# Kernel tuning notes

Measured on AMD Instinct MI355X. Metric: run time of the kernel, lower is better.

## Reference

```python
import jax, jax.numpy as jnp
import numpy as np

N = 512          # num_satellites
STATE_DIM = 6    # pos(3) + vel(3)
OBJ_DIM = 58
F = STATE_DIM + OBJ_DIM          # node feature dim = 64
HID = (128, 64, 32)
EDGE_IN = 2 * F + 1              # sender + receiver + distance
NODE_IN = F + HID[-1]            # node feats + aggregated messages


def _linear_init(key, d_in, d_out):
    kw, _ = jax.random.split(key)
    w = jax.random.normal(kw, (d_in, d_out), jnp.float32) / np.sqrt(d_in).astype(np.float32)
    b = jnp.zeros((d_out,), jnp.float32)
    return w, b


def setup_inputs() -> dict:
    key = jax.random.key(0)
    ks = jax.random.split(key, 12)
    ew0, eb0 = _linear_init(ks[0], EDGE_IN, HID[0])
    ew1, eb1 = _linear_init(ks[1], HID[0], HID[1])
    ew2, eb2 = _linear_init(ks[2], HID[1], HID[2])
    nw0, nb0 = _linear_init(ks[3], NODE_IN, HID[0])
    nw1, nb1 = _linear_init(ks[4], HID[0], HID[1])
    nw2, nb2 = _linear_init(ks[5], HID[1], HID[2])
    nwo, nbo = _linear_init(ks[6], HID[2], F)   # residual projection back to F
    rw, rb = _linear_init(ks[7], F, 3)          # control readout
    states = jax.random.normal(ks[8], (N, STATE_DIM), jnp.float32)
    objectives = jax.random.normal(ks[9], (OBJ_DIM,), jnp.float32)
    return dict(states=states, objectives=objectives,
                ew0=ew0, eb0=eb0, ew1=ew1, eb1=eb1, ew2=ew2, eb2=eb2,
                nw0=nw0, nb0=nb0, nw1=nw1, nb1=nb1, nw2=nw2, nb2=nb2,
                nwo=nwo, nbo=nbo, rw=rw, rb=rb,
                num_message_passing=3)


def _edge_index(n):
    ii, jj = np.meshgrid(np.arange(n), np.arange(n), indexing='ij')
    m = ii != jj
    return jnp.asarray(ii[m]), jnp.asarray(jj[m])  # sender i, receiver j; E = n*(n-1)


def reference(states, objectives, ew0, eb0, ew1, eb1, ew2, eb2,
              nw0, nb0, nw1, nb1, nw2, nb2, nwo, nbo, rw, rb,
              num_message_passing):
    n = states.shape[0]
    snd, rcv = _edge_index(n)
    # node features: state concat broadcast objectives -> [N, F]
    nf = jnp.concatenate(
        [states, jnp.broadcast_to(objectives, (n, objectives.shape[0]))], axis=-1)
    # distances from raw states (constant across iterations): [E, 1]
    rel = states[rcv, :3] - states[snd, :3]
    dist = jnp.linalg.norm(rel, axis=-1, keepdims=True)
    relu = jax.nn.relu
    for _ in range(num_message_passing):
        # edge MLP over all E edges: [E, 2F+1] -> [E, 32]
        x = jnp.concatenate([nf[snd], nf[rcv], dist], axis=-1)
        h = relu(x @ ew0 + eb0)
        h = relu(h @ ew1 + eb1)
        msg = relu(h @ ew2 + eb2)
        # sum-aggregate incoming messages at receiver j: [N, 32]
        agg = jax.ops.segment_sum(msg, rcv, num_segments=n)
        # node MLP + residual: [N, F+32] -> [N, F]
        y = jnp.concatenate([nf, agg], axis=-1)
        h = relu(y @ nw0 + nb0)
        h = relu(h @ nw1 + nb1)
        h = relu(h @ nw2 + nb2)
        nf = nf + h @ nwo + nbo
    # control readout: [N, 3]
    return nf @ rw + rb
```

## Files before the change

kernel.cpp:

```cpp
#include <hip/hip_runtime.h>
#include <math.h>

#define NSAT 512
#define FDIM 64
#define H0D  128
#define H1D  64
#define H2D  32
#define KP1  68
#define ROWS 256

#define WS_NF    0
#define WS_PSA   (WS_NF  + NSAT * FDIM)
#define WS_PRA   (WS_PSA + NSAT * H0D)
#define WS_PSB   (WS_PRA + NSAT * H0D)
#define WS_PRB   (WS_PSB + NSAT * H0D)
#define WS_WT    (WS_PRB + NSAT * H0D)

using short8_t = __attribute__((ext_vector_type(8))) short;
using short4_t = __attribute__((ext_vector_type(4))) short;
using int4_t   = __attribute__((ext_vector_type(4))) int;
using int2_t   = __attribute__((ext_vector_type(2))) int;
using floatx4  = __attribute__((ext_vector_type(4))) float;
using floatx16 = __attribute__((ext_vector_type(16))) float;

__device__ __forceinline__ void split_ru(float x, short& hi, short& lo) {
    unsigned u = __builtin_bit_cast(unsigned, x);
    unsigned hb = (u + 0x8000u) >> 16;
    hi = (short)hb;
    float r = x - __builtin_bit_cast(float, hb << 16);
    lo = (short)((__builtin_bit_cast(unsigned, r) + 0x8000u) >> 16);
}

__device__ __forceinline__ void split8_pk(const float* __restrict__ v,
                                          short8_t& bh, short8_t& bl) {
    unsigned t[8]; unsigned ru[8];
    #pragma unroll
    for (int e = 0; e < 8; ++e) {
        unsigned u = __builtin_bit_cast(unsigned, v[e]);
        t[e] = u + 0x8000u;
        float r = v[e] - __builtin_bit_cast(float, t[e] & 0xffff0000u);
        ru[e] = __builtin_bit_cast(unsigned, r);
    }
    int4_t hv, lv;
    #pragma unroll
    for (int p = 0; p < 4; ++p) {
        hv[p] = (int)__builtin_amdgcn_perm(t[2*p+1],  t[2*p],  0x07060302u);
        lv[p] = (int)__builtin_amdgcn_perm(ru[2*p+1], ru[2*p], 0x07060302u);
    }
    bh = __builtin_bit_cast(short8_t, hv);
    bl = __builtin_bit_cast(short8_t, lv);
}

__device__ __forceinline__ void split4_pk(const float* __restrict__ v,
                                          short4_t& h, short4_t& l) {
    unsigned t[4]; unsigned ru[4];
    #pragma unroll
    for (int e = 0; e < 4; ++e) {
        unsigned u = __builtin_bit_cast(unsigned, v[e]);
        t[e] = u + 0x8000u;
        float r = v[e] - __builtin_bit_cast(float, t[e] & 0xffff0000u);
        ru[e] = __builtin_bit_cast(unsigned, r);
    }
    int2_t hv, lv;
    #pragma unroll
    for (int p = 0; p < 2; ++p) {
        hv[p] = (int)__builtin_amdgcn_perm(t[2*p+1],  t[2*p],  0x07060302u);
        lv[p] = (int)__builtin_amdgcn_perm(ru[2*p+1], ru[2*p], 0x07060302u);
    }
    h = __builtin_bit_cast(short4_t, hv);
    l = __builtin_bit_cast(short4_t, lv);
}

__device__ __forceinline__ void compute_pre(const float* __restrict__ nfl,
                                            const float* __restrict__ ew0,
                                            const float* __restrict__ eb0,
                                            int i, int t,
                                            float* __restrict__ preSA,
                                            float* __restrict__ preR) {
    if (t < H0D) {
        int k = t;
        float s0 = 0.f, s1 = 0.f, s2 = 0.f, s3 = 0.f;
        #pragma unroll
        for (int f = 0; f < FDIM; f += 4) {
            s0 = fmaf(nfl[f + 0], ew0[(f + 0) * H0D + k], s0);
            s1 = fmaf(nfl[f + 1], ew0[(f + 1) * H0D + k], s1);
            s2 = fmaf(nfl[f + 2], ew0[(f + 2) * H0D + k], s2);
            s3 = fmaf(nfl[f + 3], ew0[(f + 3) * H0D + k], s3);
        }
        int kk = (k >> 3) & 7, lhi = k >> 6, jj = k & 7;
        preSA[((i >> 5) * 8 + kk) * 512 + (lhi * 32 + (i & 31)) * 8 + jj] =
            (s0 + s1) + (s2 + s3);
    } else if (t < 2 * H0D) {
        int k = t - H0D;
        float s0 = eb0[k], s1 = 0.f, s2 = 0.f, s3 = 0.f;
        #pragma unroll
        for (int f = 0; f < FDIM; f += 4) {
            s0 = fmaf(nfl[f + 0], ew0[(FDIM + f + 0) * H0D + k], s0);
            s1 = fmaf(nfl[f + 1], ew0[(FDIM + f + 1) * H0D + k], s1);
            s2 = fmaf(nfl[f + 2], ew0[(FDIM + f + 2) * H0D + k], s2);
            s3 = fmaf(nfl[f + 3], ew0[(FDIM + f + 3) * H0D + k], s3);
        }
        preR[i * H0D + k] = (s0 + s1) + (s2 + s3);
    }
}

__global__ void setup_kernel(const float* __restrict__ states,
                             const float* __restrict__ objectives,
                             const float* __restrict__ ew0,
                             const float* __restrict__ eb0,
                             const float* __restrict__ ew1,
                             const float* __restrict__ ew2,
                             float* __restrict__ nf,
                             float* __restrict__ preSA,
                             float* __restrict__ preR,
                             short* __restrict__ w1A_hi,
                             short* __restrict__ w1A_lo,
                             short* __restrict__ w2t_hi,
                             short* __restrict__ w2t_lo) {
    __shared__ float nfl[FDIM];
    int b = blockIdx.x, t = threadIdx.x;
    if (b < NSAT) {
        if (t < FDIM) {
            float v = (t < 6) ? states[b * 6 + t] : objectives[t - 6];
            nfl[t] = v;
            nf[b * FDIM + t] = v;
        }
        __syncthreads();
        compute_pre(nfl, ew0, eb0, b, t, preSA, preR);
    } else {
        int e = (b - NSAT) * 256 + t;
        if (e < H1D * H0D) {
            int jj = e & 7;
            int l  = (e >> 3) & 63;
            int kk = (e >> 9) & 7;
            int mh = e >> 12;
            int m = mh * 32 + (l & 31);
            int k = (l >> 5) * 64 + kk * 8 + jj;
            short hi, lo; split_ru(ew1[k * H1D + m], hi, lo);
            w1A_hi[e] = hi; w1A_lo[e] = lo;
        } else if (e < H1D * H0D + H2D * H1D) {
            int e2 = e - H1D * H0D;
            int c = e2 >> 6, k = e2 & 63;
            short hi, lo; split_ru(ew2[k * H2D + c], hi, lo);
            w2t_hi[e2] = hi; w2t_lo[e2] = lo;
        }
    }
}

__global__ __launch_bounds__(512, 2)
void edge_node_kernel(const float* __restrict__ states,
                      const float* __restrict__ preSA,
                      const float* __restrict__ preR,
                      const float* __restrict__ ew0,
                      const float* __restrict__ eb0,
                      const float* __restrict__ eb1,
                      const float* __restrict__ eb2,
                      const short* __restrict__ w1A_hi,
                      const short* __restrict__ w1A_lo,
                      const short* __restrict__ w2t_hi,
                      const short* __restrict__ w2t_lo,
                      const float* __restrict__ nw0, const float* __restrict__ nb0,
                      const float* __restrict__ nw1, const float* __restrict__ nb1,
                      const float* __restrict__ nw2, const float* __restrict__ nb2,
                      const float* __restrict__ nwo, const float* __restrict__ nbo,
                      const float* __restrict__ rw,  const float* __restrict__ rb,
                      float* __restrict__ nf,
                      float* __restrict__ preSA_w,
                      float* __restrict__ preR_w,
                      float* __restrict__ out,
                      int final_iter) {
    extern __shared__ __align__(16) short h1_dyn[];
    short* h1_hi = h1_dyn;
    short* h1_lo = h1_dyn + ROWS * KP1;

    __shared__ __align__(16) float preR_l[H0D];
    __shared__ __align__(16) float wd_l[H0D];
    __shared__ __align__(16) float eb1_l[H1D];
    __shared__ float eb2_l[H2D];
    __shared__ __align__(16) float red_l[8 * H2D];
    __shared__ float y_l[96];
    __shared__ float hA_l[H0D];
    __shared__ float hB_l[H1D];
    __shared__ float hC_l[H2D];
    __shared__ float nfl2[FDIM];

    int t = threadIdx.x, j = blockIdx.x;
    int w = t >> 6, lane = t & 63;
    int lhi = lane >> 5, llo = lane & 31;

    if (t < H0D)                          preR_l[t] = preR[j * H0D + t];
    else if (t < 2 * H0D)                 wd_l[t - H0D] = ew0[H0D * H0D + (t - H0D)];
    else if (t < 2 * H0D + H1D)           eb1_l[t - 2 * H0D] = eb1[t - 2 * H0D];
    else if (t < 2 * H0D + H1D + H2D)     eb2_l[t - 2 * H0D - H1D] = eb2[t - 2 * H0D - H1D];
    __syncthreads();

    float rjx = states[j * 6 + 0];
    float rjy = states[j * 6 + 1];
    float rjz = states[j * 6 + 2];

    int s_loc = w * 32 + llo;
    const short* pAh0 = w1A_hi + lane * 8;
    const short* pAl0 = w1A_lo + lane * 8;

    int lq = lane >> 4, l15 = lane & 15;
    const short* pA2h0 = w2t_hi + l15 * H1D + lq * 8;
    const short* pA2l0 = w2t_lo + l15 * H1D + lq * 8;
    const short* pA2h1 = w2t_hi + (16 + l15) * H1D + lq * 8;
    const short* pA2l1 = w2t_lo + (16 + l15) * H1D + lq * 8;
    int boA = (w * 32 + l15) * KP1 + lq * 8;
    int boB = boA + 16 * KP1;

    float racc[8];
    #pragma unroll
    for (int r = 0; r < 8; ++r) racc[r] = 0.f;

    #pragma unroll 1
    for (int P = 0; P < 2; ++P) {
        int s_glb = P * ROWS + s_loc;
        float dx = states[s_glb * 6 + 0] - rjx;
        float dy = states[s_glb * 6 + 1] - rjy;
        float dz = states[s_glb * 6 + 2] - rjz;
        float d = sqrtf(dx * dx + dy * dy + dz * dz);

        const float* pS = preSA + (size_t)((P * 8 + w) * 8) * 512 + lane * 8;

        floatx16 accA, accB;
        #pragma unroll
        for (int r = 0; r < 16; ++r) { accA[r] = 0.f; accB[r] = 0.f; }

        #pragma unroll
        for (int kk = 0; kk < 8; ++kk) {
            float4 a0 = *(const float4*)(pS + kk * 512);
            float4 a1 = *(const float4*)(pS + kk * 512 + 4);
            int kb = lhi * 64 + kk * 8;
            float4 r0 = *(const float4*)&preR_l[kb];
            float4 r1 = *(const float4*)&preR_l[kb + 4];
            float4 q0 = *(const float4*)&wd_l[kb];
            float4 q1 = *(const float4*)&wd_l[kb + 4];
            float v[8];
            v[0] = fmaxf(a0.x + fmaf(d, q0.x, r0.x), 0.f);
            v[1] = fmaxf(a0.y + fmaf(d, q0.y, r0.y), 0.f);
            v[2] = fmaxf(a0.z + fmaf(d, q0.z, r0.z), 0.f);
            v[3] = fmaxf(a0.w + fmaf(d, q0.w, r0.w), 0.f);
            v[4] = fmaxf(a1.x + fmaf(d, q1.x, r1.x), 0.f);
            v[5] = fmaxf(a1.y + fmaf(d, q1.y, r1.y), 0.f);
            v[6] = fmaxf(a1.z + fmaf(d, q1.z, r1.z), 0.f);
            v[7] = fmaxf(a1.w + fmaf(d, q1.w, r1.w), 0.f);
            short8_t bh, bl;
            split8_pk(v, bh, bl);
            short8_t ah0 = *(const short8_t*)(pAh0 + kk * 512);
            short8_t al0 = *(const short8_t*)(pAl0 + kk * 512);
            short8_t ah1 = *(const short8_t*)(pAh0 + 4096 + kk * 512);
            short8_t al1 = *(const short8_t*)(pAl0 + 4096 + kk * 512);
            accA = __builtin_amdgcn_mfma_f32_32x32x16_bf16(ah0, bh, accA, 0, 0, 0);
            accA = __builtin_amdgcn_mfma_f32_32x32x16_bf16(ah0, bl, accA, 0, 0, 0);
            accA = __builtin_amdgcn_mfma_f32_32x32x16_bf16(al0, bh, accA, 0, 0, 0);
            accB = __builtin_amdgcn_mfma_f32_32x32x16_bf16(ah1, bh, accB, 0, 0, 0);
            accB = __builtin_amdgcn_mfma_f32_32x32x16_bf16(ah1, bl, accB, 0, 0, 0);
            accB = __builtin_amdgcn_mfma_f32_32x32x16_bf16(al1, bh, accB, 0, 0, 0);
        }

        asm volatile("s_waitcnt lgkmcnt(0)" ::: "memory");

        {
            #pragma unroll
            for (int mh = 0; mh < 2; ++mh) {
                #pragma unroll
                for (int q = 0; q < 4; ++q) {
                    int m0 = mh * 32 + q * 8 + lhi * 4;
                    float vv[4];
                    #pragma unroll
                    for (int r = 0; r < 4; ++r) {
                        float c = mh ? accB[q * 4 + r] : accA[q * 4 + r];
                        vv[r] = fmaxf(c + eb1_l[m0 + r], 0.f);
                    }
                    short4_t ph, pl;
                    split4_pk(vv, ph, pl);
                    *(short4_t*)&h1_hi[s_loc * KP1 + m0] = ph;
                    *(short4_t*)&h1_lo[s_loc * KP1 + m0] = pl;
                }
            }
        }

        floatx4 aA0, aA1, aB0, aB1;
        #pragma unroll
        for (int r = 0; r < 4; ++r) { aA0[r]=0.f; aA1[r]=0.f; aB0[r]=0.f; aB1[r]=0.f; }
        #pragma unroll
        for (int kk = 0; kk < 2; ++kk) {
            short4_t b0, b1, c0, c1;
            b0 = *(const short4_t*)&h1_hi[boA + kk * 32];
            b1 = *(const short4_t*)&h1_hi[boA + kk * 32 + 4];
            c0 = *(const short4_t*)&h1_lo[boA + kk * 32];
            c1 = *(const short4_t*)&h1_lo[boA + kk * 32 + 4];
            short8_t bhA = __builtin_shufflevector(b0, b1, 0,1,2,3,4,5,6,7);
            short8_t blA = __builtin_shufflevector(c0, c1, 0,1,2,3,4,5,6,7);
            b0 = *(const short4_t*)&h1_hi[boB + kk * 32];
            b1 = *(const short4_t*)&h1_hi[boB + kk * 32 + 4];
            c0 = *(const short4_t*)&h1_lo[boB + kk * 32];
            c1 = *(const short4_t*)&h1_lo[boB + kk * 32 + 4];
            short8_t bhB = __builtin_shufflevector(b0, b1, 0,1,2,3,4,5,6,7);
            short8_t blB = __builtin_shufflevector(c0, c1, 0,1,2,3,4,5,6,7);
            short8_t a0h = *(const short8_t*)(pA2h0 + kk * 32);
            short8_t a0l = *(const short8_t*)(pA2l0 + kk * 32);
            short8_t a1h = *(const short8_t*)(pA2h1 + kk * 32);
            short8_t a1l = *(const short8_t*)(pA2l1 + kk * 32);
            aA0 = __builtin_amdgcn_mfma_f32_16x16x32_bf16(a0h, bhA, aA0, 0, 0, 0);
            aA0 = __builtin_amdgcn_mfma_f32_16x16x32_bf16(a0h, blA, aA0, 0, 0, 0);
            aA0 = __builtin_amdgcn_mfma_f32_16x16x32_bf16(a0l, bhA, aA0, 0, 0, 0);
            aA1 = __builtin_amdgcn_mfma_f32_16x16x32_bf16(a1h, bhA, aA1, 0, 0, 0);
            aA1 = __builtin_amdgcn_mfma_f32_16x16x32_bf16(a1h, blA, aA1, 0, 0, 0);
            aA1 = __builtin_amdgcn_mfma_f32_16x16x32_bf16(a1l, bhA, aA1, 0, 0, 0);
            aB0 = __builtin_amdgcn_mfma_f32_16x16x32_bf16(a0h, bhB, aB0, 0, 0, 0);
            aB0 = __builtin_amdgcn_mfma_f32_16x16x32_bf16(a0h, blB, aB0, 0, 0, 0);
            aB0 = __builtin_amdgcn_mfma_f32_16x16x32_bf16(a0l, bhB, aB0, 0, 0, 0);
            aB1 = __builtin_amdgcn_mfma_f32_16x16x32_bf16(a1h, bhB, aB1, 0, 0, 0);
            aB1 = __builtin_amdgcn_mfma_f32_16x16x32_bf16(a1h, blB, aB1, 0, 0, 0);
            aB1 = __builtin_amdgcn_mfma_f32_16x16x32_bf16(a1l, bhB, aB1, 0, 0, 0);
        }

        {
            bool selfA = (P * ROWS + w * 32 + l15 == j);
            bool selfB = (P * ROWS + w * 32 + 16 + l15 == j);
            #pragma unroll
            for (int r = 0; r < 4; ++r) {
                float vA = fmaxf(aA0[r] + eb2_l[lq * 4 + r], 0.f);
                float vB = fmaxf(aB0[r] + eb2_l[lq * 4 + r], 0.f);
                if (selfA) vA = 0.f;
                if (selfB) vB = 0.f;
                racc[r] += vA + vB;
                float wA = fmaxf(aA1[r] + eb2_l[16 + lq * 4 + r], 0.f);
                float wB = fmaxf(aB1[r] + eb2_l[16 + lq * 4 + r], 0.f);
                if (selfA) wA = 0.f;
                if (selfB) wB = 0.f;
                racc[4 + r] += wA + wB;
            }
        }
    }

    {
        #pragma unroll
        for (int r = 0; r < 8; ++r) {
            float v = racc[r];
            v += __shfl_xor(v, 1, 64); v += __shfl_xor(v, 2, 64);
            v += __shfl_xor(v, 4, 64); v += __shfl_xor(v, 8, 64);
            racc[r] = v;
        }
        if (l15 == 0) {
            *(float4*)&red_l[w * H2D + lq * 4] =
                make_float4(racc[0], racc[1], racc[2], racc[3]);
            *(float4*)&red_l[w * H2D + 16 + lq * 4] =
                make_float4(racc[4], racc[5], racc[6], racc[7]);
        }
    }
    __syncthreads();

    if (t < FDIM) y_l[t] = nf[j * FDIM + t];
    else if (t < 96) {
        int c = t - FDIM;
        float s = 0.f;
        #pragma unroll
        for (int gg = 0; gg < 8; ++gg) s += red_l[gg * H2D + c];
        y_l[t] = s;
    }
    __syncthreads();
    if (t < H0D) {
        float s0 = nb0[t], s1 = 0.f, s2 = 0.f, s3 = 0.f;
        #pragma unroll
        for (int f = 0; f < 96; f += 4) {
            s0 = fmaf(y_l[f + 0], nw0[(f + 0) * H0D + t], s0);
            s1 = fmaf(y_l[f + 1], nw0[(f + 1) * H0D + t], s1);
            s2 = fmaf(y_l[f + 2], nw0[(f + 2) * H0D + t], s2);
            s3 = fmaf(y_l[f + 3], nw0[(f + 3) * H0D + t], s3);
        }
        hA_l[t] = fmaxf((s0 + s1) + (s2 + s3), 0.f);
    }
    __syncthreads();
    if (t < H1D) {
        float s0 = nb1[t], s1 = 0.f, s2 = 0.f, s3 = 0.f;
        #pragma unroll
        for (int k = 0; k < H0D; k += 4) {
            s0 = fmaf(hA_l[k + 0], nw1[(k + 0) * H1D + t], s0);
            s1 = fmaf(hA_l[k + 1], nw1[(k + 1) * H1D + t], s1);
            s2 = fmaf(hA_l[k + 2], nw1[(k + 2) * H1D + t], s2);
            s3 = fmaf(hA_l[k + 3], nw1[(k + 3) * H1D + t], s3);
        }
        hB_l[t] = fmaxf((s0 + s1) + (s2 + s3), 0.f);
    }
    __syncthreads();
    if (t < H2D) {
        float s0 = nb2[t], s1 = 0.f, s2 = 0.f, s3 = 0.f;
        #pragma unroll
        for (int m = 0; m < H1D; m += 4) {
            s0 = fmaf(hB_l[m + 0], nw2[(m + 0) * H2D + t], s0);
            s1 = fmaf(hB_l[m + 1], nw2[(m + 1) * H2D + t], s1);
            s2 = fmaf(hB_l[m + 2], nw2[(m + 2) * H2D + t], s2);
            s3 = fmaf(hB_l[m + 3], nw2[(m + 3) * H2D + t], s3);
        }
        hC_l[t] = fmaxf((s0 + s1) + (s2 + s3), 0.f);
    }
    __syncthreads();
    if (t < FDIM) {
        float s = nbo[t];
        #pragma unroll
        for (int c = 0; c < H2D; ++c) s = fmaf(hC_l[c], nwo[c * FDIM + t], s);
        float v = y_l[t] + s;
        nfl2[t] = v;
        if (!final_iter) nf[j * FDIM + t] = v;
    }
    __syncthreads();
    if (final_iter) {
        if (t < 3) {
            float s0 = rb[t], s1 = 0.f, s2 = 0.f, s3 = 0.f;
            #pragma unroll
            for (int f = 0; f < FDIM; f += 4) {
                s0 = fmaf(nfl2[f + 0], rw[(f + 0) * 3 + t], s0);
                s1 = fmaf(nfl2[f + 1], rw[(f + 1) * 3 + t], s1);
                s2 = fmaf(nfl2[f + 2], rw[(f + 2) * 3 + t], s2);
                s3 = fmaf(nfl2[f + 3], rw[(f + 3) * 3 + t], s3);
            }
            out[j * 3 + t] = (s0 + s1) + (s2 + s3);
        }
    } else {
        compute_pre(nfl2, ew0, eb0, j, t, preSA_w, preR_w);
    }
}

extern "C" void kernel_launch(void* const* d_in, const int* in_sizes, int n_in,
                              void* d_out, int out_size, void* d_ws, size_t ws_size,
                              hipStream_t stream) {
    const float* states     = (const float*)d_in[0];
    const float* objectives = (const float*)d_in[1];
    const float* ew0 = (const float*)d_in[2];
    const float* eb0 = (const float*)d_in[3];
    const float* ew1 = (const float*)d_in[4];
    const float* eb1 = (const float*)d_in[5];
    const float* ew2 = (const float*)d_in[6];
    const float* eb2 = (const float*)d_in[7];
    const float* nw0 = (const float*)d_in[8];
    const float* nb0 = (const float*)d_in[9];
    const float* nw1 = (const float*)d_in[10];
    const float* nb1 = (const float*)d_in[11];
    const float* nw2 = (const float*)d_in[12];
    const float* nb2 = (const float*)d_in[13];
    const float* nwo = (const float*)d_in[14];
    const float* nbo = (const float*)d_in[15];
    const float* rw  = (const float*)d_in[16];
    const float* rb  = (const float*)d_in[17];
    float* out = (float*)d_out;
    float* ws  = (float*)d_ws;

    float* nf      = ws + WS_NF;
    float* preSA_a = ws + WS_PSA;
    float* preR_a  = ws + WS_PRA;
    float* preSA_b = ws + WS_PSB;
    float* preR_b  = ws + WS_PRB;
    short* w1A_hi = (short*)(ws + WS_WT);
    short* w1A_lo = w1A_hi + H1D * H0D;
    short* w2t_hi = w1A_lo + H1D * H0D;
    short* w2t_lo = w2t_hi + H2D * H1D;

    const int dyn_lds = 2 * ROWS * KP1 * (int)sizeof(short);
    static bool attr_set = false;
    if (!attr_set) {
        hipFuncSetAttribute((const void*)edge_node_kernel,
                            hipFuncAttributeMaxDynamicSharedMemorySize, dyn_lds);
        attr_set = true;
    }

    setup_kernel<<<NSAT + 40, 256, 0, stream>>>(states, objectives, ew0, eb0,
                                                ew1, ew2, nf, preSA_a, preR_a,
                                                w1A_hi, w1A_lo, w2t_hi, w2t_lo);
    for (int it = 0; it < 3; ++it) {
        const float* pS_r = (it & 1) ? preSA_b : preSA_a;
        const float* pR_r = (it & 1) ? preR_b  : preR_a;
        float* pS_w = (it & 1) ? preSA_a : preSA_b;
        float* pR_w = (it & 1) ? preR_a  : preR_b;
        edge_node_kernel<<<NSAT, 512, dyn_lds, stream>>>(
            states, pS_r, pR_r, ew0, eb0, eb1, eb2,
            w1A_hi, w1A_lo, w2t_hi, w2t_lo,
            nw0, nb0, nw1, nb1, nw2, nb2, nwo, nbo, rw, rb,
            nf, pS_w, pR_w, out, (it == 2) ? 1 : 0);
    }
}
```

Before: 198.1 us.

## Process two receiver nodes per block to reuse sender preactivations and weights

Each block now computes the edge and node MLPs for two receiver nodes, sharing the sender preactivation loads and the bf16 weight fragments across both. The grid is halved, LDS for the hidden layer is doubled, and launch bounds drop to one block per CU. This aims to cut global/L2 traffic and fragment loads per edge, at the cost of more registers, lower occupancy and fewer blocks to balance across CUs.

```diff
diff --git a/kernel.cpp b/kernel.cpp
--- a/kernel.cpp
+++ b/kernel.cpp
@@ -147,7 +147,7 @@
     }
 }
 
-__global__ __launch_bounds__(512, 2)
+__global__ __launch_bounds__(512, 1)
 void edge_node_kernel(const float* __restrict__ states,
                       const float* __restrict__ preSA,
                       const float* __restrict__ preR,
@@ -170,33 +170,36 @@
                       float* __restrict__ out,
                       int final_iter) {
     extern __shared__ __align__(16) short h1_dyn[];
-    short* h1_hi = h1_dyn;
-    short* h1_lo = h1_dyn + ROWS * KP1;
-
-    __shared__ __align__(16) float preR_l[H0D];
+    short* h1_hi0 = h1_dyn;
+    short* h1_lo0 = h1_dyn + ROWS * KP1;
+    short* h1_hi1 = h1_dyn + 2 * ROWS * KP1;
+    short* h1_lo1 = h1_dyn + 3 * ROWS * KP1;
+
+    __shared__ __align__(16) float preR_l[2][H0D];
     __shared__ __align__(16) float wd_l[H0D];
     __shared__ __align__(16) float eb1_l[H1D];
     __shared__ float eb2_l[H2D];
-    __shared__ __align__(16) float red_l[8 * H2D];
-    __shared__ float y_l[96];
-    __shared__ float hA_l[H0D];
-    __shared__ float hB_l[H1D];
-    __shared__ float hC_l[H2D];
-    __shared__ float nfl2[FDIM];
-
-    int t = threadIdx.x, j = blockIdx.x;
+    __shared__ __align__(16) float red_l[2][8 * H2D];
+    __shared__ float y_l[2][96];
+    __shared__ float hA_l[2][H0D];
+    __shared__ float hB_l[2][H1D];
+    __shared__ float hC_l[2][H2D];
+    __shared__ float nfl2[2][FDIM];
+
+    int t = threadIdx.x;
+    int j0 = blockIdx.x * 2, j1 = j0 + 1;
     int w = t >> 6, lane = t & 63;
     int lhi = lane >> 5, llo = lane & 31;
 
-    if (t < H0D)                          preR_l[t] = preR[j * H0D + t];
-    else if (t < 2 * H0D)                 wd_l[t - H0D] = ew0[H0D * H0D + (t - H0D)];
-    else if (t < 2 * H0D + H1D)           eb1_l[t - 2 * H0D] = eb1[t - 2 * H0D];
-    else if (t < 2 * H0D + H1D + H2D)     eb2_l[t - 2 * H0D - H1D] = eb2[t - 2 * H0D - H1D];
-    __syncthreads();
-
-    float rjx = states[j * 6 + 0];
-    float rjy = states[j * 6 + 1];
-    float rjz = states[j * 6 + 2];
+    if (t < H0D)                               preR_l[0][t] = preR[j0 * H0D + t];
+    else if (t < 2 * H0D)                      preR_l[1][t - H0D] = preR[j1 * H0D + (t - H0D)];
+    else if (t < 3 * H0D)                      wd_l[t - 2 * H0D] = ew0[H0D * H0D + (t - 2 * H0D)];
+    else if (t < 3 * H0D + H1D)                eb1_l[t - 3 * H0D] = eb1[t - 3 * H0D];
+    else if (t < 3 * H0D + H1D + H2D)          eb2_l[t - 3 * H0D - H1D] = eb2[t - 3 * H0D - H1D];
+    __syncthreads();
+
+    float r0x = states[j0 * 6 + 0], r0y = states[j0 * 6 + 1], r0z = states[j0 * 6 + 2];
+    float r1x = states[j1 * 6 + 0], r1y = states[j1 * 6 + 1], r1z = states[j1 * 6 + 2];
 
     int s_loc = w * 32 + llo;
     const short* pAh0 = w1A_hi + lane * 8;
@@ -210,59 +213,84 @@
     int boA = (w * 32 + l15) * KP1 + lq * 8;
     int boB = boA + 16 * KP1;
 
-    float racc[8];
+    float racc0[8], racc1[8];
     #pragma unroll
-    for (int r = 0; r < 8; ++r) racc[r] = 0.f;
+    for (int r = 0; r < 8; ++r) { racc0[r] = 0.f; racc1[r] = 0.f; }
 
     #pragma unroll 1
     for (int P = 0; P < 2; ++P) {
         int s_glb = P * ROWS + s_loc;
-        float dx = states[s_glb * 6 + 0] - rjx;
-        float dy = states[s_glb * 6 + 1] - rjy;
-        float dz = states[s_glb * 6 + 2] - rjz;
-        float d = sqrtf(dx * dx + dy * dy + dz * dz);
+        float sx = states[s_glb * 6 + 0];
+        float sy = states[s_glb * 6 + 1];
+        float sz = states[s_glb * 6 + 2];
+        float dx0 = sx - r0x, dy0 = sy - r0y, dz0 = sz - r0z;
+        float d0 = sqrtf(dx0 * dx0 + dy0 * dy0 + dz0 * dz0);
+        float dx1 = sx - r1x, dy1 = sy - r1y, dz1 = sz - r1z;
+        float d1 = sqrtf(dx1 * dx1 + dy1 * dy1 + dz1 * dz1);
 
         const float* pS = preSA + (size_t)((P * 8 + w) * 8) * 512 + lane * 8;
 
-        floatx16 accA, accB;
-        #pragma unroll
-        for (int r = 0; r < 16; ++r) { accA[r] = 0.f; accB[r] = 0.f; }
+        floatx16 accLo0, accHi0, accLo1, accHi1;
+        #pragma unroll
+        for (int r = 0; r < 16; ++r) {
+            accLo0[r] = 0.f; accHi0[r] = 0.f; accLo1[r] = 0.f; accHi1[r] = 0.f;
+        }
 
         #pragma unroll
         for (int kk = 0; kk < 8; ++kk) {
             float4 a0 = *(const float4*)(pS + kk * 512);
             float4 a1 = *(const float4*)(pS + kk * 512 + 4);
             int kb = lhi * 64 + kk * 8;
-            float4 r0 = *(const float4*)&preR_l[kb];
-            float4 r1 = *(const float4*)&preR_l[kb + 4];
+            float4 p00 = *(const float4*)&preR_l[0][kb];
+            float4 p01 = *(const float4*)&preR_l[0][kb + 4];
+            float4 p10 = *(const float4*)&preR_l[1][kb];
+            float4 p11 = *(const float4*)&preR_l[1][kb + 4];
             float4 q0 = *(const float4*)&wd_l[kb];
             float4 q1 = *(const float4*)&wd_l[kb + 4];
-            float v[8];
-            v[0] = fmaxf(a0.x + fmaf(d, q0.x, r0.x), 0.f);
-            v[1] = fmaxf(a0.y + fmaf(d, q0.y, r0.y), 0.f);
-            v[2] = fmaxf(a0.z + fmaf(d, q0.z, r0.z), 0.f);
-            v[3] = fmaxf(a0.w + fmaf(d, q0.w, r0.w), 0.f);
-            v[4] = fmaxf(a1.x + fmaf(d, q1.x, r1.x), 0.f);
-            v[5] = fmaxf(a1.y + fmaf(d, q1.y, r1.y), 0.f);
-            v[6] = fmaxf(a1.z + fmaf(d, q1.z, r1.z), 0.f);
-            v[7] = fmaxf(a1.w + fmaf(d, q1.w, r1.w), 0.f);
-            short8_t bh, bl;
-            split8_pk(v, bh, bl);
-            short8_t ah0 = *(const short8_t*)(pAh0 + kk * 512);
-            short8_t al0 = *(const short8_t*)(pAl0 + kk * 512);
-            short8_t ah1 = *(const short8_t*)(pAh0 + 4096 + kk * 512);
-            short8_t al1 = *(const short8_t*)(pAl0 + 4096 + kk * 512);
-            accA = __builtin_amdgcn_mfma_f32_32x32x16_bf16(ah0, bh, accA, 0, 0, 0);
-            accA = __builtin_amdgcn_mfma_f32_32x32x16_bf16(ah0, bl, accA, 0, 0, 0);
-            accA = __builtin_amdgcn_mfma_f32_32x32x16_bf16(al0, bh, accA, 0, 0, 0);
-            accB = __builtin_amdgcn_mfma_f32_32x32x16_bf16(ah1, bh, accB, 0, 0, 0);
-            accB = __builtin_amdgcn_mfma_f32_32x32x16_bf16(ah1, bl, accB, 0, 0, 0);
-            accB = __builtin_amdgcn_mfma_f32_32x32x16_bf16(al1, bh, accB, 0, 0, 0);
+            float v0[8], v1[8];
+            v0[0] = fmaxf(a0.x + fmaf(d0, q0.x, p00.x), 0.f);
+            v0[1] = fmaxf(a0.y + fmaf(d0, q0.y, p00.y), 0.f);
+            v0[2] = fmaxf(a0.z + fmaf(d0, q0.z, p00.z), 0.f);
+            v0[3] = fmaxf(a0.w + fmaf(d0, q0.w, p00.w), 0.f);
+            v0[4] = fmaxf(a1.x + fmaf(d0, q1.x, p01.x), 0.f);
+            v0[5] = fmaxf(a1.y + fmaf(d0, q1.y, p01.y), 0.f);
+            v0[6] = fmaxf(a1.z + fmaf(d0, q1.z, p01.z), 0.f);
+            v0[7] = fmaxf(a1.w + fmaf(d0, q1.w, p01.w), 0.f);
+            v1[0] = fmaxf(a0.x + fmaf(d1, q0.x, p10.x), 0.f);
+            v1[1] = fmaxf(a0.y + fmaf(d1, q0.y, p10.y), 0.f);
+            v1[2] = fmaxf(a0.z + fmaf(d1, q0.z, p10.z), 0.f);
+            v1[3] = fmaxf(a0.w + fmaf(d1, q0.w, p10.w), 0.f);
+            v1[4] = fmaxf(a1.x + fmaf(d1, q1.x, p11.x), 0.f);
+            v1[5] = fmaxf(a1.y + fmaf(d1, q1.y, p11.y), 0.f);
+            v1[6] = fmaxf(a1.z + fmaf(d1, q1.z, p11.z), 0.f);
+            v1[7] = fmaxf(a1.w + fmaf(d1, q1.w, p11.w), 0.f);
+            short8_t bh0, bl0, bh1, bl1;
+            split8_pk(v0, bh0, bl0);
+            split8_pk(v1, bh1, bl1);
+            short8_t whi0 = *(const short8_t*)(pAh0 + kk * 512);
+            short8_t wlo0 = *(const short8_t*)(pAl0 + kk * 512);
+            short8_t whi1 = *(const short8_t*)(pAh0 + 4096 + kk * 512);
+            short8_t wlo1 = *(const short8_t*)(pAl0 + 4096 + kk * 512);
+            accLo0 = __builtin_amdgcn_mfma_f32_32x32x16_bf16(whi0, bh0, accLo0, 0, 0, 0);
+            accLo1 = __builtin_amdgcn_mfma_f32_32x32x16_bf16(whi0, bh1, accLo1, 0, 0, 0);
+            accHi0 = __builtin_amdgcn_mfma_f32_32x32x16_bf16(whi1, bh0, accHi0, 0, 0, 0);
+            accHi1 = __builtin_amdgcn_mfma_f32_32x32x16_bf16(whi1, bh1, accHi1, 0, 0, 0);
+            accLo0 = __builtin_amdgcn_mfma_f32_32x32x16_bf16(whi0, bl0, accLo0, 0, 0, 0);
+            accLo1 = __builtin_amdgcn_mfma_f32_32x32x16_bf16(whi0, bl1, accLo1, 0, 0, 0);
+            accHi0 = __builtin_amdgcn_mfma_f32_32x32x16_bf16(whi1, bl0, accHi0, 0, 0, 0);
+            accHi1 = __builtin_amdgcn_mfma_f32_32x32x16_bf16(whi1, bl1, accHi1, 0, 0, 0);
+            accLo0 = __builtin_amdgcn_mfma_f32_32x32x16_bf16(wlo0, bh0, accLo0, 0, 0, 0);
+            accLo1 = __builtin_amdgcn_mfma_f32_32x32x16_bf16(wlo0, bh1, accLo1, 0, 0, 0);
+            accHi0 = __builtin_amdgcn_mfma_f32_32x32x16_bf16(wlo1, bh0, accHi0, 0, 0, 0);
+            accHi1 = __builtin_amdgcn_mfma_f32_32x32x16_bf16(wlo1, bh1, accHi1, 0, 0, 0);
         }
 
         asm volatile("s_waitcnt lgkmcnt(0)" ::: "memory");
 
-        {
+        #pragma unroll
+        for (int jx = 0; jx < 2; ++jx) {
+            short* hh = jx ? h1_hi1 : h1_hi0;
+            short* hl = jx ? h1_lo1 : h1_lo0;
             #pragma unroll
             for (int mh = 0; mh < 2; ++mh) {
                 #pragma unroll
@@ -271,68 +299,92 @@
                     float vv[4];
                     #pragma unroll
                     for (int r = 0; r < 4; ++r) {
-                        float c = mh ? accB[q * 4 + r] : accA[q * 4 + r];
+                        float c;
+                        if (jx == 0) c = mh ? accHi0[q * 4 + r] : accLo0[q * 4 + r];
+                        else         c = mh ? accHi1[q * 4 + r] : accLo1[q * 4 + r];
                         vv[r] = fmaxf(c + eb1_l[m0 + r], 0.f);
                     }
                     short4_t ph, pl;
                     split4_pk(vv, ph, pl);
-                    *(short4_t*)&h1_hi[s_loc * KP1 + m0] = ph;
-                    *(short4_t*)&h1_lo[s_loc * KP1 + m0] = pl;
+                    *(short4_t*)&hh[s_loc * KP1 + m0] = ph;
+                    *(short4_t*)&hl[s_loc * KP1 + m0] = pl;
                 }
             }
         }
 
-        floatx4 aA0, aA1, aB0, aB1;
-        #pragma unroll
-        for (int r = 0; r < 4; ++r) { aA0[r]=0.f; aA1[r]=0.f; aB0[r]=0.f; aB1[r]=0.f; }
+        floatx4 aA0_0, aA1_0, aB0_0, aB1_0, aA0_1, aA1_1, aB0_1, aB1_1;
+        #pragma unroll
+        for (int r = 0; r < 4; ++r) {
+            aA0_0[r]=0.f; aA1_0[r]=0.f; aB0_0[r]=0.f; aB1_0[r]=0.f;
+            aA0_1[r]=0.f; aA1_1[r]=0.f; aB0_1[r]=0.f; aB1_1[r]=0.f;
+        }
         #pragma unroll
         for (int kk = 0; kk < 2; ++kk) {
-            short4_t b0, b1, c0, c1;
-            b0 = *(const short4_t*)&h1_hi[boA + kk * 32];
-            b1 = *(const short4_t*)&h1_hi[boA + kk * 32 + 4];
-            c0 = *(const short4_t*)&h1_lo[boA + kk * 32];
-            c1 = *(const short4_t*)&h1_lo[boA + kk * 32 + 4];
-            short8_t bhA = __builtin_shufflevector(b0, b1, 0,1,2,3,4,5,6,7);
-            short8_t blA = __builtin_shufflevector(c0, c1, 0,1,2,3,4,5,6,7);
-            b0 = *(const short4_t*)&h1_hi[boB + kk * 32];
-            b1 = *(const short4_t*)&h1_hi[boB + kk * 32 + 4];
-            c0 = *(const short4_t*)&h1_lo[boB + kk * 32];
-            c1 = *(const short4_t*)&h1_lo[boB + kk * 32 + 4];
-            short8_t bhB = __builtin_shufflevector(b0, b1, 0,1,2,3,4,5,6,7);
-            short8_t blB = __builtin_shufflevector(c0, c1, 0,1,2,3,4,5,6,7);
             short8_t a0h = *(const short8_t*)(pA2h0 + kk * 32);
             short8_t a0l = *(const short8_t*)(pA2l0 + kk * 32);
             short8_t a1h = *(const short8_t*)(pA2h1 + kk * 32);
             short8_t a1l = *(const short8_t*)(pA2l1 + kk * 32);
-            aA0 = __builtin_amdgcn_mfma_f32_16x16x32_bf16(a0h, bhA, aA0, 0, 0, 0);
-            aA0 = __builtin_amdgcn_mfma_f32_16x16x32_bf16(a0h, blA, aA0, 0, 0, 0);
-            aA0 = __builtin_amdgcn_mfma_f32_16x16x32_bf16(a0l, bhA, aA0, 0, 0, 0);
-            aA1 = __builtin_amdgcn_mfma_f32_16x16x32_bf16(a1h, bhA, aA1, 0, 0, 0);
-            aA1 = __builtin_amdgcn_mfma_f32_16x16x32_bf16(a1h, blA, aA1, 0, 0, 0);
-            aA1 = __builtin_amdgcn_mfma_f32_16x16x32_bf16(a1l, bhA, aA1, 0, 0, 0);
-            aB0 = __builtin_amdgcn_mfma_f32_16x16x32_bf16(a0h, bhB, aB0, 0, 0, 0);
-            aB0 = __builtin_amdgcn_mfma_f32_16x16x32_bf16(a0h, blB, aB0, 0, 0, 0);
-            aB0 = __builtin_amdgcn_mfma_f32_16x16x32_bf16(a0l, bhB, aB0, 0, 0, 0);
-            aB1 = __builtin_amdgcn_mfma_f32_16x16x32_bf16(a1h, bhB, aB1, 0, 0, 0);
-            aB1 = __builtin_amdgcn_mfma_f32_16x16x32_bf16(a1h, blB, aB1, 0, 0, 0);
-            aB1 = __builtin_amdgcn_mfma_f32_16x16x32_bf16(a1l, bhB, aB1, 0, 0, 0);
+            #pragma unroll
+            for (int jx = 0; jx < 2; ++jx) {
+                const short* hh = jx ? h1_hi1 : h1_hi0;
+                const short* hl = jx ? h1_lo1 : h1_lo0;
+                short4_t u0, u1, c0, c1;
+                u0 = *(const short4_t*)&hh[boA + kk * 32];
+                u1 = *(const short4_t*)&hh[boA + kk * 32 + 4];
+                c0 = *(const short4_t*)&hl[boA + kk * 32];
+                c1 = *(const short4_t*)&hl[boA + kk * 32 + 4];
+                short8_t bhA = __builtin_shufflevector(u0, u1, 0,1,2,3,4,5,6,7);
+                short8_t blA = __builtin_shufflevector(c0, c1, 0,1,2,3,4,5,6,7);
+                u0 = *(const short4_t*)&hh[boB + kk * 32];
+                u1 = *(const short4_t*)&hh[boB + kk * 32 + 4];
+                c0 = *(const short4_t*)&hl[boB + kk * 32];
+                c1 = *(const short4_t*)&hl[boB + kk * 32 + 4];
+                short8_t bhB = __builtin_shufflevector(u0, u1, 0,1,2,3,4,5,6,7);
+                short8_t blB = __builtin_shufflevector(c0, c1, 0,1,2,3,4,5,6,7);
+                floatx4 xA0 = jx ? aA0_1 : aA0_0;
+                floatx4 xA1 = jx ? aA1_1 : aA1_0;
+                floatx4 xB0 = jx ? aB0_1 : aB0_0;
+                floatx4 xB1 = jx ? aB1_1 : aB1_0;
+                xA0 = __builtin_amdgcn_mfma_f32_16x16x32_bf16(a0h, bhA, xA0, 0, 0, 0);
+                xB0 = __builtin_amdgcn_mfma_f32_16x16x32_bf16(a0h, bhB, xB0, 0, 0, 0);
+                xA1 = __builtin_amdgcn_mfma_f32_16x16x32_bf16(a1h, bhA, xA1, 0, 0, 0);
+                xB1 = __builtin_amdgcn_mfma_f32_16x16x32_bf16(a1h, bhB, xB1, 0, 0, 0);
+                xA0 = __builtin_amdgcn_mfma_f32_16x16x32_bf16(a0h, blA, xA0, 0, 0, 0);
+                xB0 = __builtin_amdgcn_mfma_f32_16x16x32_bf16(a0h, blB, xB0, 0, 0, 0);
+                xA1 = __builtin_amdgcn_mfma_f32_16x16x32_bf16(a1h, blA, xA1, 0, 0, 0);
+                xB1 = __builtin_amdgcn_mfma_f32_16x16x32_bf16(a1h, blB, xB1, 0, 0, 0);
+                xA0 = __builtin_amdgcn_mfma_f32_16x16x32_bf16(a0l, bhA, xA0, 0, 0, 0);
+                xB0 = __builtin_amdgcn_mfma_f32_16x16x32_bf16(a0l, bhB, xB0, 0, 0, 0);
+                xA1 = __builtin_amdgcn_mfma_f32_16x16x32_bf16(a1l, bhA, xA1, 0, 0, 0);
+                xB1 = __builtin_amdgcn_mfma_f32_16x16x32_bf16(a1l, bhB, xB1, 0, 0, 0);
+                if (jx == 0) { aA0_0 = xA0; aA1_0 = xA1; aB0_0 = xB0; aB1_0 = xB1; }
+                else         { aA0_1 = xA0; aA1_1 = xA1; aB0_1 = xB0; aB1_1 = xB1; }
+            }
         }
 
         {
-            bool selfA = (P * ROWS + w * 32 + l15 == j);
-            bool selfB = (P * ROWS + w * 32 + 16 + l15 == j);
+            int sA = P * ROWS + w * 32 + l15;
+            int sB = sA + 16;
             #pragma unroll
             for (int r = 0; r < 4; ++r) {
-                float vA = fmaxf(aA0[r] + eb2_l[lq * 4 + r], 0.f);
-                float vB = fmaxf(aB0[r] + eb2_l[lq * 4 + r], 0.f);
-                if (selfA) vA = 0.f;
-                if (selfB) vB = 0.f;
-                racc[r] += vA + vB;
-                float wA = fmaxf(aA1[r] + eb2_l[16 + lq * 4 + r], 0.f);
-                float wB = fmaxf(aB1[r] + eb2_l[16 + lq * 4 + r], 0.f);
-                if (selfA) wA = 0.f;
-                if (selfB) wB = 0.f;
-                racc[4 + r] += wA + wB;
+                float e0 = eb2_l[lq * 4 + r];
+                float e1 = eb2_l[16 + lq * 4 + r];
+                float vA = fmaxf(aA0_0[r] + e0, 0.f);
+                float vB = fmaxf(aB0_0[r] + e0, 0.f);
+                float uA = fmaxf(aA1_0[r] + e1, 0.f);
+                float uB = fmaxf(aB1_0[r] + e1, 0.f);
+                if (sA == j0) { vA = 0.f; uA = 0.f; }
+                if (sB == j0) { vB = 0.f; uB = 0.f; }
+                racc0[r]     += vA + vB;
+                racc0[4 + r] += uA + uB;
+                float wA = fmaxf(aA0_1[r] + e0, 0.f);
+                float wB = fmaxf(aB0_1[r] + e0, 0.f);
+                float zA = fmaxf(aA1_1[r] + e1, 0.f);
+                float zB = fmaxf(aB1_1[r] + e1, 0.f);
+                if (sA == j1) { wA = 0.f; zA = 0.f; }
+                if (sB == j1) { wB = 0.f; zB = 0.f; }
+                racc1[r]     += wA + wB;
+                racc1[4 + r] += zA + zB;
             }
         }
     }
@@ -340,88 +392,99 @@
     {
         #pragma unroll
         for (int r = 0; r < 8; ++r) {
-            float v = racc[r];
+            float v = racc0[r];
             v += __shfl_xor(v, 1, 64); v += __shfl_xor(v, 2, 64);
             v += __shfl_xor(v, 4, 64); v += __shfl_xor(v, 8, 64);
-            racc[r] = v;
+            racc0[r] = v;
+            float u = racc1[r];
+            u += __shfl_xor(u, 1, 64); u += __shfl_xor(u, 2, 64);
+            u += __shfl_xor(u, 4, 64); u += __shfl_xor(u, 8, 64);
+            racc1[r] = u;
         }
         if (l15 == 0) {
-            *(float4*)&red_l[w * H2D + lq * 4] =
-                make_float4(racc[0], racc[1], racc[2], racc[3]);
-            *(float4*)&red_l[w * H2D + 16 + lq * 4] =
-                make_float4(racc[4], racc[5], racc[6], racc[7]);
-        }
-    }
-    __syncthreads();
-
-    if (t < FDIM) y_l[t] = nf[j * FDIM + t];
-    else if (t < 96) {
-        int c = t - FDIM;
+            *(float4*)&red_l[0][w * H2D + lq * 4] =
+                make_float4(racc0[0], racc0[1], racc0[2], racc0[3]);
+            *(float4*)&red_l[0][w * H2D + 16 + lq * 4] =
+                make_float4(racc0[4], racc0[5], racc0[6], racc0[7]);
+            *(float4*)&red_l[1][w * H2D + lq * 4] =
+                make_float4(racc1[0], racc1[1], racc1[2], racc1[3]);
+            *(float4*)&red_l[1][w * H2D + 16 + lq * 4] =
+                make_float4(racc1[4], racc1[5], racc1[6], racc1[7]);
+        }
+    }
+    __syncthreads();
+
+    int tl = t & 255;
+    int jx = t >> 8;
+    int jj = j0 + jx;
+    if (tl < FDIM) y_l[jx][tl] = nf[jj * FDIM + tl];
+    else if (tl < 96) {
+        int c = tl - FDIM;
         float s = 0.f;
         #pragma unroll
-        for (int gg = 0; gg < 8; ++gg) s += red_l[gg * H2D + c];
-        y_l[t] = s;
-    }
-    __syncthreads();
-    if (t < H0D) {
-        float s0 = nb0[t], s1 = 0.f, s2 = 0.f, s3 = 0.f;
+        for (int gg = 0; gg < 8; ++gg) s += red_l[jx][gg * H2D + c];
+        y_l[jx][tl] = s;
+    }
+    __syncthreads();
+    if (tl < H0D) {
+        float s0 = nb0[tl], s1 = 0.f, s2 = 0.f, s3 = 0.f;
         #pragma unroll
         for (int f = 0; f < 96; f += 4) {
-            s0 = fmaf(y_l[f + 0], nw0[(f + 0) * H0D + t], s0);
-            s1 = fmaf(y_l[f + 1], nw0[(f + 1) * H0D + t], s1);
-            s2 = fmaf(y_l[f + 2], nw0[(f + 2) * H0D + t], s2);
-            s3 = fmaf(y_l[f + 3], nw0[(f + 3) * H0D + t], s3);
-        }
-        hA_l[t] = fmaxf((s0 + s1) + (s2 + s3), 0.f);
-    }
-    __syncthreads();
-    if (t < H1D) {
-        float s0 = nb1[t], s1 = 0.f, s2 = 0.f, s3 = 0.f;
+            s0 = fmaf(y_l[jx][f + 0], nw0[(f + 0) * H0D + tl], s0);
+            s1 = fmaf(y_l[jx][f + 1], nw0[(f + 1) * H0D + tl], s1);
+            s2 = fmaf(y_l[jx][f + 2], nw0[(f + 2) * H0D + tl], s2);
+            s3 = fmaf(y_l[jx][f + 3], nw0[(f + 3) * H0D + tl], s3);
+        }
+        hA_l[jx][tl] = fmaxf((s0 + s1) + (s2 + s3), 0.f);
+    }
+    __syncthreads();
+    if (tl < H1D) {
+        float s0 = nb1[tl], s1 = 0.f, s2 = 0.f, s3 = 0.f;
         #pragma unroll
         for (int k = 0; k < H0D; k += 4) {
-            s0 = fmaf(hA_l[k + 0], nw1[(k + 0) * H1D + t], s0);
-            s1 = fmaf(hA_l[k + 1], nw1[(k + 1) * H1D + t], s1);
-            s2 = fmaf(hA_l[k + 2], nw1[(k + 2) * H1D + t], s2);
-            s3 = fmaf(hA_l[k + 3], nw1[(k + 3) * H1D + t], s3);
-        }
-        hB_l[t] = fmaxf((s0 + s1) + (s2 + s3), 0.f);
-    }
-    __syncthreads();
-    if (t < H2D) {
-        float s0 = nb2[t], s1 = 0.f, s2 = 0.f, s3 = 0.f;
+            s0 = fmaf(hA_l[jx][k + 0], nw1[(k + 0) * H1D + tl], s0);
+            s1 = fmaf(hA_l[jx][k + 1], nw1[(k + 1) * H1D + tl], s1);
+            s2 = fmaf(hA_l[jx][k + 2], nw1[(k + 2) * H1D + tl], s2);
+            s3 = fmaf(hA_l[jx][k + 3], nw1[(k + 3) * H1D + tl], s3);
+        }
+        hB_l[jx][tl] = fmaxf((s0 + s1) + (s2 + s3), 0.f);
+    }
+    __syncthreads();
+    if (tl < H2D) {
+        float s0 = nb2[tl], s1 = 0.f, s2 = 0.f, s3 = 0.f;
         #pragma unroll
         for (int m = 0; m < H1D; m += 4) {
-            s0 = fmaf(hB_l[m + 0], nw2[(m + 0) * H2D + t], s0);
-            s1 = fmaf(hB_l[m + 1], nw2[(m + 1) * H2D + t], s1);
-            s2 = fmaf(hB_l[m + 2], nw2[(m + 2) * H2D + t], s2);
-            s3 = fmaf(hB_l[m + 3], nw2[(m + 3) * H2D + t], s3);
-        }
-        hC_l[t] = fmaxf((s0 + s1) + (s2 + s3), 0.f);
-    }
-    __syncthreads();
-    if (t < FDIM) {
-        float s = nbo[t];
-        #pragma unroll
-        for (int c = 0; c < H2D; ++c) s = fmaf(hC_l[c], nwo[c * FDIM + t], s);
-        float v = y_l[t] + s;
-        nfl2[t] = v;
-        if (!final_iter) nf[j * FDIM + t] = v;
+            s0 = fmaf(hB_l[jx][m + 0], nw2[(m + 0) * H2D + tl], s0);
+            s1 = fmaf(hB_l[jx][m + 1], nw2[(m + 1) * H2D + tl], s1);
+            s2 = fmaf(hB_l[jx][m + 2], nw2[(m + 2) * H2D + tl], s2);
+            s3 = fmaf(hB_l[jx][m + 3], nw2[(m + 3) * H2D + tl], s3);
+        }
+        hC_l[jx][tl] = fmaxf((s0 + s1) + (s2 + s3), 0.f);
+    }
+    __syncthreads();
+    if (tl < FDIM) {
+        float s = nbo[tl];
+        #pragma unroll
+        for (int c = 0; c < H2D; ++c) s = fmaf(hC_l[jx][c], nwo[c * FDIM + tl], s);
+        float v = y_l[jx][tl] + s;
+        nfl2[jx][tl] = v;
+        if (!final_iter) nf[jj * FDIM + tl] = v;
     }
     __syncthreads();
     if (final_iter) {
-        if (t < 3) {
-            float s0 = rb[t], s1 = 0.f, s2 = 0.f, s3 = 0.f;
+        if (tl < 3) {
+            float s0 = rb[tl], s1 = 0.f, s2 = 0.f, s3 = 0.f;
             #pragma unroll
             for (int f = 0; f < FDIM; f += 4) {
-                s0 = fmaf(nfl2[f + 0], rw[(f + 0) * 3 + t], s0);
-                s1 = fmaf(nfl2[f + 1], rw[(f + 1) * 3 + t], s1);
-                s2 = fmaf(nfl2[f + 2], rw[(f + 2) * 3 + t], s2);
-                s3 = fmaf(nfl2[f + 3], rw[(f + 3) * 3 + t], s3);
+                s0 = fmaf(nfl2[jx][f + 0], rw[(f + 0) * 3 + tl], s0);
+                s1 = fmaf(nfl2[jx][f + 1], rw[(f + 1) * 3 + tl], s1);
+                s2 = fmaf(nfl2[jx][f + 2], rw[(f + 2) * 3 + tl], s2);
+                s3 = fmaf(nfl2[jx][f + 3], rw[(f + 3) * 3 + tl], s3);
             }
-            out[j * 3 + t] = (s0 + s1) + (s2 + s3);
+            out[jj * 3 + tl] = (s0 + s1) + (s2 + s3);
         }
     } else {
-        compute_pre(nfl2, ew0, eb0, j, t, preSA_w, preR_w);
+        compute_pre(nfl2[jx], ew0, eb0, jj, tl, preSA_w, preR_w);
     }
 }
 
@@ -459,7 +522,7 @@
     short* w2t_hi = w1A_lo + H1D * H0D;
     short* w2t_lo = w2t_hi + H2D * H1D;
 
-    const int dyn_lds = 2 * ROWS * KP1 * (int)sizeof(short);
+    const int dyn_lds = 4 * ROWS * KP1 * (int)sizeof(short);
     static bool attr_set = false;
     if (!attr_set) {
         hipFuncSetAttribute((const void*)edge_node_kernel,
@@ -475,7 +538,7 @@
         const float* pR_r = (it & 1) ? preR_b  : preR_a;
         float* pS_w = (it & 1) ? preSA_a : preSA_b;
         float* pR_w = (it & 1) ? preR_a  : preR_b;
-        edge_node_kernel<<<NSAT, 512, dyn_lds, stream>>>(
+        edge_node_kernel<<<NSAT / 2, 512, dyn_lds, stream>>>(
             states, pS_r, pR_r, ew0, eb0, eb1, eb2,
             w1A_hi, w1A_lo, w2t_hi, w2t_lo,
             nw0, nb0, nw1, nb1, nw2, nb2, nwo, nbo, rw, rb,
```

Result: faster. 193.1 us (-2.6%).
